# Optimization experiments

Measured on AMD Instinct MI355X. Metric: run time of the kernel, lower is better.

The kernel has to match this reference:

```python
import math
import jax, jax.numpy as jnp
import numpy as np

NLAT, NLON = 61, 120
C, H = 64, 4
DH = C // H
HID = 128
NSEG = NLAT * NLON  # number of grid points / softmax segments
EPS = 1e-6
SCALE = 1.0 / math.sqrt(DH)


def _build_geometry():
    """Neighbor pairs within theta_cutoff on the equiangular (pole-including) grid.

    The neighborhood structure is longitude-shift invariant, so we enumerate it
    for output longitude 0 and replicate with a modular longitude shift.
    """
    nlat, nlon = NLAT, NLON
    theta = np.pi * np.arange(nlat) / (nlat - 1)           # colatitudes incl. poles
    lam = 2.0 * np.pi * np.arange(nlon) / nlon
    theta_cutoff = 7.0 / math.sqrt(math.pi) * math.pi / (nlat - 1)
    ct, st = np.cos(theta), np.sin(theta)
    # great-circle distance between (theta_o, 0) and (theta_i, dlon): [nlat, nlat, nlon]
    cosd = (ct[:, None, None] * ct[None, :, None]
            + st[:, None, None] * st[None, :, None] * np.cos(lam)[None, None, :])
    dist = np.arccos(np.clip(cosd, -1.0, 1.0))
    ho, hi, dl = np.nonzero(dist <= theta_cutoff)          # E reference-column entries
    wo = np.arange(nlon)
    out_idx = (ho[:, None] * nlon + wo[None, :]).reshape(-1).astype(np.int32)
    in_idx = (hi[:, None] * nlon + (dl[:, None] + wo[None, :]) % nlon).reshape(-1).astype(np.int32)
    # quadrature (integration) weights: sin(theta) measure, zero at the poles
    w = (st * (np.pi / (nlat - 1)) * (2.0 * np.pi / nlon)).astype(np.float32)
    quad_w = np.repeat(w, nlon)                            # [NSEG]
    return jnp.asarray(out_idx), jnp.asarray(in_idx), jnp.asarray(quad_w)


def setup_inputs() -> dict:
    key = jax.random.key(0)
    ks = jax.random.split(key, 8)
    out_idx, in_idx, quad_w = _build_geometry()

    def w(k, shape, fan_in):
        return jax.random.normal(k, shape, dtype=jnp.float32) / np.float32(np.sqrt(fan_in))

    return {
        "x": jax.random.normal(ks[0], (1, C, NLAT, NLON), dtype=jnp.float32),
        "wq": w(ks[1], (C, C), C),
        "wk": w(ks[2], (C, C), C),
        "wv": w(ks[3], (C, C), C),
        "wo": w(ks[4], (C, C), C),
        "w1": w(ks[5], (HID, C), C),
        "b1": jnp.zeros((HID,), jnp.float32),
        "w2": w(ks[6], (C, HID), HID),
        "b2": jnp.zeros((C,), jnp.float32),
        "ln0_g": jnp.ones((C,), jnp.float32),
        "ln0_b": jnp.zeros((C,), jnp.float32),
        "ln1_g": jnp.ones((C,), jnp.float32),
        "ln1_b": jnp.zeros((C,), jnp.float32),
        "quad_w": quad_w,
        "out_idx": out_idx,
        "in_idx": in_idx,
    }


def _layernorm(x, g, b):
    # channel-wise LayerNorm at every spatial location; x: [B, C, H, W]
    m = jnp.mean(x, axis=1, keepdims=True)
    v = jnp.mean((x - m) ** 2, axis=1, keepdims=True)
    xh = (x - m) * jax.lax.rsqrt(v + EPS)
    return xh * g[None, :, None, None] + b[None, :, None, None]


def _neighborhood_attn(x, wq, wk, wv, wo, quad_w, out_idx, in_idx):
    # x: [B, C, nlat, nlon] (fp32)
    B = x.shape[0]
    q = jnp.einsum('oc,bchw->bohw', wq, x).reshape(B, H, DH, NSEG)
    k = jnp.einsum('oc,bchw->bohw', wk, x).reshape(B, H, DH, NSEG)
    v = jnp.einsum('oc,bchw->bohw', wv, x).reshape(B, H, DH, NSEG)
    qg = q[..., out_idx]                                   # [B,H,DH,NNZ]
    kg = k[..., in_idx]
    s = jnp.einsum('bhdn,bhdn->bhn', qg, kg) * SCALE       # [B,H,NNZ]
    s = jnp.moveaxis(s, -1, 0)                             # [NNZ,B,H]
    smax = jax.ops.segment_max(s, out_idx, num_segments=NSEG)
    # quadrature-weighted, numerically stable softmax over each neighborhood
    alpha = jnp.exp(s - smax[out_idx]) * quad_w[in_idx][:, None, None]
    vg = jnp.moveaxis(v[..., in_idx], -1, 0)               # [NNZ,B,H,DH]
    num = jax.ops.segment_sum(alpha[..., None] * vg, out_idx, num_segments=NSEG)
    den = jax.ops.segment_sum(alpha, out_idx, num_segments=NSEG)
    att = num / den[..., None]                             # [NSEG,B,H,DH]
    att = jnp.moveaxis(att, 0, -1).reshape(B, C, NLAT, NLON)
    return jnp.einsum('oc,bchw->bohw', wo, att)


def reference(x, wq, wk, wv, wo, w1, b1, w2, b2, ln0_g, ln0_b, ln1_g, ln1_b,
              quad_w, out_idx, in_idx):
    residual = x
    h0 = _layernorm(x, ln0_g, ln0_b)
    a = _neighborhood_attn(h0.astype(jnp.float32), wq, wk, wv, wo,
                           quad_w, out_idx, in_idx).astype(x.dtype)
    x1 = a + residual
    h1 = _layernorm(x1, ln1_g, ln1_b)
    m = jax.nn.gelu(jnp.einsum('fc,bchw->bfhw', w1, h1) + b1[None, :, None, None],
                    approximate=False)
    m = jnp.einsum('cf,bfhw->bchw', w2, m) + b2[None, :, None, None]
    return m + x1
```

## Files before the change

kernel.cpp:

```cpp
#include <hip/hip_runtime.h>
#include <math.h>

#define NSEG 7320
#define NLON 120
#define HIDN 128
#define ECH  16
#define MAXCH 48

__global__ __launch_bounds__(64) void k1_ln_qkv(
    const float* __restrict__ x,  const float* __restrict__ wq,
    const float* __restrict__ wk, const float* __restrict__ wv,
    const float* __restrict__ g,  const float* __restrict__ b,
    const int* __restrict__ out_idx, const int* __restrict__ in_idx,
    const float* __restrict__ qw, int E,
    float* __restrict__ q_pl, float* __restrict__ k_pl, float* __restrict__ v_pl,
    int* __restrict__ row_start, int4* __restrict__ meta,
    float4* __restrict__ zbase)
{
    const int lane = threadIdx.x;
    const int tile = blockIdx.x;
    const int grp  = blockIdx.y;

    if (grp >= 25) {
        const int n4 = (68 * NSEG) / 4;
        for (int i = ((grp - 25) * 115 + tile) * 64 + lane; i < n4; i += 2 * 115 * 64)
            zbase[i] = make_float4(0.f, 0.f, 0.f, 0.f);
        return;
    }
    if (grp == 24) {
        for (int e = tile * 64 + lane; e < E; e += 115 * 64) {
            int ho = out_idx[e * NLON] / NLON;
            if (e == 0) {
                row_start[ho] = 0;
            } else {
                int hp = out_idx[(e - 1) * NLON] / NLON;
                if (hp != ho) row_start[ho] = e;
            }
            if (e == E - 1) row_start[ho + 1] = E;
            int i0 = in_idx[e * NLON];
            int hi = i0 / NLON;
            int dl = i0 - hi * NLON;
            meta[e] = make_int4(hi * NLON, dl, __float_as_int(qw[i0]), ho);
        }
        return;
    }

    const int n = tile * 64 + lane;
    if (n >= NSEG) return;

    float xv[64];
    float s = 0.f, s2 = 0.f;
#pragma unroll
    for (int c = 0; c < 64; ++c) { float t = x[c * NSEG + n]; xv[c] = t; s += t; s2 += t * t; }
    float mean = s * 0.015625f;
    float var  = s2 * 0.015625f - mean * mean;
    float rstd = rsqrtf(var + 1e-6f);
#pragma unroll
    for (int c = 0; c < 64; ++c) xv[c] = (xv[c] - mean) * rstd * g[c] + b[c];

    const int mm    = grp >> 3;
    const int obase = (grp & 7) * 8;
    const float* __restrict__ w = (mm == 0) ? wq : (mm == 1) ? wk : wv;
    float* __restrict__ dst = (mm == 0) ? q_pl : (mm == 1) ? k_pl : v_pl;
    const float scale = (mm == 0) ? 0.25f : 1.0f;

#pragma unroll
    for (int j = 0; j < 8; ++j) {
        int o = obase + j;
        float acc = 0.f;
#pragma unroll
        for (int c = 0; c < 64; ++c) acc += w[o * 64 + c] * xv[c];
        dst[o * NSEG + n] = acc * scale;
    }
}

__global__ __launch_bounds__(128) void k2_attn(
    const float* __restrict__ q_pl, const float* __restrict__ k_pl,
    const float* __restrict__ v_pl,
    const int4* __restrict__ meta,  const int* __restrict__ row_start,
    float* __restrict__ num, float* __restrict__ den)
{
    const int wo  = threadIdx.x;
    const bool aw = wo < NLON;
    const int woc = aw ? wo : (NLON - 1);
    const int ho  = blockIdx.x;
    const int head = blockIdx.z;
    const int cb  = head * 16;

    int e0 = __builtin_amdgcn_readfirstlane(row_start[ho]);
    int e1 = __builtin_amdgcn_readfirstlane(row_start[ho + 1]);
    int eb = e0 + blockIdx.y * ECH;
    if (eb >= e1) return;
    int ee = eb + ECH; if (ee > e1) ee = e1;

    const int segc = ho * NLON + woc;
    const float* __restrict__ qb = q_pl + (size_t)cb * NSEG;
    const float* __restrict__ kb = k_pl + (size_t)cb * NSEG;
    const float* __restrict__ vb = v_pl + (size_t)cb * NSEG;

    float qreg[16];
#pragma unroll
    for (int c = 0; c < 16; ++c) qreg[c] = qb[c * NSEG + segc];

    float acc[16];
#pragma unroll
    for (int c = 0; c < 16; ++c) acc[c] = 0.f;
    float dh = 0.f;

#pragma unroll 2
    for (int e = eb; e < ee; ++e) {
        int4 mt = meta[e];
        int dlw = mt.y + woc; if (dlw >= NLON) dlw -= NLON;
        const float* __restrict__ kp = kb + (mt.x + dlw);
        const float* __restrict__ vp = vb + (mt.x + dlw);

        float sa = 0.f, sb = 0.f;
#pragma unroll
        for (int c = 0; c < 8; ++c)  sa += qreg[c]     * kp[c * NSEG];
#pragma unroll
        for (int c = 0; c < 8; ++c)  sb += qreg[8 + c] * kp[(8 + c) * NSEG];

        float qwv = aw ? __int_as_float(mt.z) : 0.f;
        float a = __expf(sa + sb) * qwv;
        dh += a;

#pragma unroll
        for (int c = 0; c < 16; ++c) acc[c] = fmaf(a, vp[c * NSEG], acc[c]);
    }

    if (aw) {
        const int seg = ho * NLON + wo;
#pragma unroll
        for (int c = 0; c < 16; ++c) atomicAdd(&num[(cb + c) * NSEG + seg], acc[c]);
        atomicAdd(&den[head * NSEG + seg], dh);
    }
}

__global__ __launch_bounds__(64) void k2c_wo(
    const float* __restrict__ num, const float* __restrict__ den,
    const float* __restrict__ wo,  const float* __restrict__ x,
    float* __restrict__ x1)
{
    const int lane = threadIdx.x;
    const int n    = blockIdx.x * 64 + lane;
    if (n >= NSEG) return;

    float rdh[4];
#pragma unroll
    for (int h = 0; h < 4; ++h) rdh[h] = 1.0f / den[h * NSEG + n];

    float att[64];
#pragma unroll
    for (int c = 0; c < 64; ++c) att[c] = num[c * NSEG + n] * rdh[c >> 4];

    const int o0 = blockIdx.y * 8;
#pragma unroll
    for (int j = 0; j < 8; ++j) {
        int o = o0 + j;
        float acc = 0.f;
#pragma unroll
        for (int c = 0; c < 64; ++c) acc += wo[o * 64 + c] * att[c];
        x1[o * NSEG + n] = acc + x[o * NSEG + n];
    }
}

__global__ __launch_bounds__(64) void k3a_mlp1(
    const float* __restrict__ x1, const float* __restrict__ w1,
    const float* __restrict__ b1, const float* __restrict__ g,
    const float* __restrict__ bb, float* __restrict__ m_act)
{
    const int lane = threadIdx.x;
    const int n    = blockIdx.x * 64 + lane;
    if (n >= NSEG) return;

    float xv[64];
    float s = 0.f, s2 = 0.f;
#pragma unroll
    for (int c = 0; c < 64; ++c) { float t = x1[c * NSEG + n]; xv[c] = t; s += t; s2 += t * t; }
    float mean = s * 0.015625f;
    float var  = s2 * 0.015625f - mean * mean;
    float rstd = rsqrtf(var + 1e-6f);
#pragma unroll
    for (int c = 0; c < 64; ++c) xv[c] = (xv[c] - mean) * rstd * g[c] + bb[c];

    const int h0 = blockIdx.y * 8;
#pragma unroll
    for (int j = 0; j < 8; ++j) {
        int h = h0 + j;
        float mh = b1[h];
#pragma unroll
        for (int c = 0; c < 64; ++c) mh += w1[h * 64 + c] * xv[c];
        m_act[h * NSEG + n] = 0.5f * mh * (1.0f + erff(mh * 0.70710678118654752f));
    }
}

__global__ __launch_bounds__(64) void k3b_mlp2(
    const float* __restrict__ m_act, const float* __restrict__ w2,
    const float* __restrict__ b2,    const float* __restrict__ x1,
    float* __restrict__ out)
{
    const int lane = threadIdx.x;
    const int n    = blockIdx.x * 64 + lane;
    if (n >= NSEG) return;
    const int c0   = blockIdx.y * 8;

    float acc[8];
#pragma unroll
    for (int j = 0; j < 8; ++j) acc[j] = 0.f;

#pragma unroll 8
    for (int h = 0; h < HIDN; ++h) {
        float mh = m_act[h * NSEG + n];
#pragma unroll
        for (int j = 0; j < 8; ++j) acc[j] += w2[(c0 + j) * HIDN + h] * mh;
    }
#pragma unroll
    for (int j = 0; j < 8; ++j) {
        int c = c0 + j;
        out[c * NSEG + n] = acc[j] + b2[c] + x1[c * NSEG + n];
    }
}

extern "C" void kernel_launch(void* const* d_in, const int* in_sizes, int n_in,
                              void* d_out, int out_size, void* d_ws, size_t ws_size,
                              hipStream_t stream)
{
    const float* x    = (const float*)d_in[0];
    const float* wq   = (const float*)d_in[1];
    const float* wk   = (const float*)d_in[2];
    const float* wv   = (const float*)d_in[3];
    const float* wo   = (const float*)d_in[4];
    const float* w1   = (const float*)d_in[5];
    const float* b1   = (const float*)d_in[6];
    const float* w2   = (const float*)d_in[7];
    const float* b2   = (const float*)d_in[8];
    const float* ln0g = (const float*)d_in[9];
    const float* ln0b = (const float*)d_in[10];
    const float* ln1g = (const float*)d_in[11];
    const float* ln1b = (const float*)d_in[12];
    const float* qw   = (const float*)d_in[13];
    const int* out_idx = (const int*)d_in[14];
    const int* in_idx  = (const int*)d_in[15];
    float* out = (float*)d_out;

    const int NNZ = in_sizes[15];
    const int E   = NNZ / NLON;
    const size_t N64 = (size_t)NSEG * 64;

    float* ws    = (float*)d_ws;
    float* q_pl  = ws;
    float* k_pl  = ws + N64;
    float* v_pl  = ws + 2 * N64;
    float* num   = ws + 3 * N64;
    float* den   = ws + 4 * N64;
    float* x1    = ws + 4 * N64 + 4 * NSEG;
    float* m_act = ws + 5 * N64 + 4 * NSEG;
    int*   row_start = (int*)(ws + 7 * N64 + 4 * NSEG);
    int4*  meta  = (int4*)(ws + 7 * N64 + 4 * NSEG + 64);

    hipLaunchKernelGGL(k1_ln_qkv, dim3(115, 27), dim3(64), 0, stream,
                       x, wq, wk, wv, ln0g, ln0b, out_idx, in_idx, qw, E,
                       q_pl, k_pl, v_pl, row_start, meta, (float4*)num);
    hipLaunchKernelGGL(k2_attn, dim3(61, MAXCH, 4), dim3(128), 0, stream,
                       q_pl, k_pl, v_pl, meta, row_start, num, den);
    hipLaunchKernelGGL(k2c_wo, dim3(115, 8), dim3(64), 0, stream,
                       num, den, wo, x, x1);
    hipLaunchKernelGGL(k3a_mlp1, dim3(115, 16), dim3(64), 0, stream,
                       x1, w1, b1, ln1g, ln1b, m_act);
    hipLaunchKernelGGL(k3b_mlp2, dim3(115, 8), dim3(64), 0, stream,
                       m_act, w2, b2, x1, out);
}
```

Baseline: 186.3 us.

## Interleave per-head Q/K/V channels for vectorized float4 neighbor gathers

Q, K and V are now stored per head as [head][point][16] instead of channel planes. The attention kernel can then gather each neighbor's key and value with four contiguous float4 loads rather than sixteen loads a full plane apart, which cuts scattered memory transactions. The QKV projection kernel now computes one whole head (16 outputs) per block, so the LayerNorm is recomputed fewer times and the grid shrinks. The maximum chunk count for the attention grid is also lowered, which assumes no latitude row has more than 576 neighbor entries.

```diff
diff --git a/kernel.cpp b/kernel.cpp
--- a/kernel.cpp
+++ b/kernel.cpp
@@ -5,7 +5,7 @@
 #define NLON 120
 #define HIDN 128
 #define ECH  16
-#define MAXCH 48
+#define MAXCH 36
 
 __global__ __launch_bounds__(64) void k1_ln_qkv(
     const float* __restrict__ x,  const float* __restrict__ wq,
@@ -13,7 +13,7 @@
     const float* __restrict__ g,  const float* __restrict__ b,
     const int* __restrict__ out_idx, const int* __restrict__ in_idx,
     const float* __restrict__ qw, int E,
-    float* __restrict__ q_pl, float* __restrict__ k_pl, float* __restrict__ v_pl,
+    float* __restrict__ q_i, float* __restrict__ k_i, float* __restrict__ v_i,
     int* __restrict__ row_start, int4* __restrict__ meta,
     float4* __restrict__ zbase)
 {
@@ -21,13 +21,13 @@
     const int tile = blockIdx.x;
     const int grp  = blockIdx.y;
 
-    if (grp >= 25) {
+    if (grp >= 13) {
         const int n4 = (68 * NSEG) / 4;
-        for (int i = ((grp - 25) * 115 + tile) * 64 + lane; i < n4; i += 2 * 115 * 64)
+        for (int i = ((grp - 13) * 115 + tile) * 64 + lane; i < n4; i += 2 * 115 * 64)
             zbase[i] = make_float4(0.f, 0.f, 0.f, 0.f);
         return;
     }
-    if (grp == 24) {
+    if (grp == 12) {
         for (int e = tile * 64 + lane; e < E; e += 115 * 64) {
             int ho = out_idx[e * NLON] / NLON;
             if (e == 0) {
@@ -58,25 +58,32 @@
 #pragma unroll
     for (int c = 0; c < 64; ++c) xv[c] = (xv[c] - mean) * rstd * g[c] + b[c];
 
-    const int mm    = grp >> 3;
-    const int obase = (grp & 7) * 8;
+    const int mm   = grp >> 2;
+    const int head = grp & 3;
     const float* __restrict__ w = (mm == 0) ? wq : (mm == 1) ? wk : wv;
-    float* __restrict__ dst = (mm == 0) ? q_pl : (mm == 1) ? k_pl : v_pl;
+    float* __restrict__ dst = (mm == 0) ? q_i : (mm == 1) ? k_i : v_i;
     const float scale = (mm == 0) ? 0.25f : 1.0f;
 
-#pragma unroll
-    for (int j = 0; j < 8; ++j) {
-        int o = obase + j;
-        float acc = 0.f;
-#pragma unroll
-        for (int c = 0; c < 64; ++c) acc += w[o * 64 + c] * xv[c];
-        dst[o * NSEG + n] = acc * scale;
-    }
+    float acc[16];
+#pragma unroll
+    for (int j = 0; j < 16; ++j) {
+        const float* __restrict__ wr = w + (head * 16 + j) * 64;
+        float a = 0.f;
+#pragma unroll
+        for (int c = 0; c < 64; ++c) a += wr[c] * xv[c];
+        acc[j] = a * scale;
+    }
+
+    float4* __restrict__ dp = (float4*)(dst + (((size_t)head * NSEG + n) << 4));
+    dp[0] = make_float4(acc[0],  acc[1],  acc[2],  acc[3]);
+    dp[1] = make_float4(acc[4],  acc[5],  acc[6],  acc[7]);
+    dp[2] = make_float4(acc[8],  acc[9],  acc[10], acc[11]);
+    dp[3] = make_float4(acc[12], acc[13], acc[14], acc[15]);
 }
 
 __global__ __launch_bounds__(128) void k2_attn(
-    const float* __restrict__ q_pl, const float* __restrict__ k_pl,
-    const float* __restrict__ v_pl,
+    const float* __restrict__ q_i, const float* __restrict__ k_i,
+    const float* __restrict__ v_i,
     const int4* __restrict__ meta,  const int* __restrict__ row_start,
     float* __restrict__ num, float* __restrict__ den)
 {
@@ -94,13 +101,12 @@
     int ee = eb + ECH; if (ee > e1) ee = e1;
 
     const int segc = ho * NLON + woc;
-    const float* __restrict__ qb = q_pl + (size_t)cb * NSEG;
-    const float* __restrict__ kb = k_pl + (size_t)cb * NSEG;
-    const float* __restrict__ vb = v_pl + (size_t)cb * NSEG;
-
-    float qreg[16];
-#pragma unroll
-    for (int c = 0; c < 16; ++c) qreg[c] = qb[c * NSEG + segc];
+    const float4* __restrict__ qp =
+        (const float4*)(q_i + (((size_t)head * NSEG + segc) << 4));
+    const float4 q0 = qp[0], q1 = qp[1], q2 = qp[2], q3 = qp[3];
+
+    const float* __restrict__ kbase = k_i + (((size_t)head * NSEG) << 4);
+    const float* __restrict__ vbase = v_i + (((size_t)head * NSEG) << 4);
 
     float acc[16];
 #pragma unroll
@@ -111,21 +117,30 @@
     for (int e = eb; e < ee; ++e) {
         int4 mt = meta[e];
         int dlw = mt.y + woc; if (dlw >= NLON) dlw -= NLON;
-        const float* __restrict__ kp = kb + (mt.x + dlw);
-        const float* __restrict__ vp = vb + (mt.x + dlw);
-
-        float sa = 0.f, sb = 0.f;
-#pragma unroll
-        for (int c = 0; c < 8; ++c)  sa += qreg[c]     * kp[c * NSEG];
-#pragma unroll
-        for (int c = 0; c < 8; ++c)  sb += qreg[8 + c] * kp[(8 + c) * NSEG];
+        const size_t poff = ((size_t)(mt.x + dlw)) << 4;
+        const float4* __restrict__ kp = (const float4*)(kbase + poff);
+        const float4* __restrict__ vp = (const float4*)(vbase + poff);
+
+        float4 ka = kp[0], kb = kp[1], kc = kp[2], kd = kp[3];
+        float sa = q0.x * ka.x; sa = fmaf(q0.y, ka.y, sa); sa = fmaf(q0.z, ka.z, sa); sa = fmaf(q0.w, ka.w, sa);
+        float sb = q1.x * kb.x; sb = fmaf(q1.y, kb.y, sb); sb = fmaf(q1.z, kb.z, sb); sb = fmaf(q1.w, kb.w, sb);
+        float sc = q2.x * kc.x; sc = fmaf(q2.y, kc.y, sc); sc = fmaf(q2.z, kc.z, sc); sc = fmaf(q2.w, kc.w, sc);
+        float sd = q3.x * kd.x; sd = fmaf(q3.y, kd.y, sd); sd = fmaf(q3.z, kd.z, sd); sd = fmaf(q3.w, kd.w, sd);
+        float sscore = (sa + sb) + (sc + sd);
 
         float qwv = aw ? __int_as_float(mt.z) : 0.f;
-        float a = __expf(sa + sb) * qwv;
+        float a = __expf(sscore) * qwv;
         dh += a;
 
-#pragma unroll
-        for (int c = 0; c < 16; ++c) acc[c] = fmaf(a, vp[c * NSEG], acc[c]);
+        float4 va = vp[0], vb = vp[1], vc = vp[2], vd = vp[3];
+        acc[0]  = fmaf(a, va.x, acc[0]);  acc[1]  = fmaf(a, va.y, acc[1]);
+        acc[2]  = fmaf(a, va.z, acc[2]);  acc[3]  = fmaf(a, va.w, acc[3]);
+        acc[4]  = fmaf(a, vb.x, acc[4]);  acc[5]  = fmaf(a, vb.y, acc[5]);
+        acc[6]  = fmaf(a, vb.z, acc[6]);  acc[7]  = fmaf(a, vb.w, acc[7]);
+        acc[8]  = fmaf(a, vc.x, acc[8]);  acc[9]  = fmaf(a, vc.y, acc[9]);
+        acc[10] = fmaf(a, vc.z, acc[10]); acc[11] = fmaf(a, vc.w, acc[11]);
+        acc[12] = fmaf(a, vd.x, acc[12]); acc[13] = fmaf(a, vd.y, acc[13]);
+        acc[14] = fmaf(a, vd.z, acc[14]); acc[15] = fmaf(a, vd.w, acc[15]);
     }
 
     if (aw) {
@@ -248,9 +263,9 @@
     const size_t N64 = (size_t)NSEG * 64;
 
     float* ws    = (float*)d_ws;
-    float* q_pl  = ws;
-    float* k_pl  = ws + N64;
-    float* v_pl  = ws + 2 * N64;
+    float* q_i   = ws;
+    float* k_i   = ws + N64;
+    float* v_i   = ws + 2 * N64;
     float* num   = ws + 3 * N64;
     float* den   = ws + 4 * N64;
     float* x1    = ws + 4 * N64 + 4 * NSEG;
@@ -258,11 +273,11 @@
     int*   row_start = (int*)(ws + 7 * N64 + 4 * NSEG);
     int4*  meta  = (int4*)(ws + 7 * N64 + 4 * NSEG + 64);
 
-    hipLaunchKernelGGL(k1_ln_qkv, dim3(115, 27), dim3(64), 0, stream,
+    hipLaunchKernelGGL(k1_ln_qkv, dim3(115, 15), dim3(64), 0, stream,
                        x, wq, wk, wv, ln0g, ln0b, out_idx, in_idx, qw, E,
-                       q_pl, k_pl, v_pl, row_start, meta, (float4*)num);
+                       q_i, k_i, v_i, row_start, meta, (float4*)num);
     hipLaunchKernelGGL(k2_attn, dim3(61, MAXCH, 4), dim3(128), 0, stream,
-                       q_pl, k_pl, v_pl, meta, row_start, num, den);
+                       q_i, k_i, v_i, meta, row_start, num, den);
     hipLaunchKernelGGL(k2c_wo, dim3(115, 8), dim3(64), 0, stream,
                        num, den, wo, x, x1);
     hipLaunchKernelGGL(k3a_mlp1, dim3(115, 16), dim3(64), 0, stream,
```

Result: slower. 216.1 us (+16.0%).
